# Kernel optimization log

Hardware: AMD Instinct MI355X
Metric: run time of the kernel (lower is better)

## Reference

```python
import jax, jax.numpy as jnp
import numpy as np

NUM_EMBEDS = 8192
EMBED_DIM = 256
BETA = 0.25


def setup_inputs() -> dict:
    key = jax.random.key(0)
    k1, k2 = jax.random.split(key)
    x_latent = jax.random.normal(k1, (16, EMBED_DIM, 32, 32), dtype=jnp.float32)
    # torch init: uniform(-1/num_embeds, 1/num_embeds)
    codebook = jax.random.uniform(
        k2, (NUM_EMBEDS, EMBED_DIM), dtype=jnp.float32,
        minval=-1.0 / NUM_EMBEDS, maxval=1.0 / NUM_EMBEDS)
    return {"x_latent": x_latent, "codebook": codebook}


def reference(x_latent, codebook):
    B, C, H, W = x_latent.shape  # C == EMBED_DIM
    # b c h w -> b (h w) c
    xf = x_latent.reshape(B, C, H * W).transpose(0, 2, 1)  # [B, N, D]
    x2 = jnp.sum(xf * xf, axis=-1, keepdims=True)            # [B, N, 1]
    e2 = jnp.sum(codebook * codebook, axis=-1)               # [E]
    xe = jnp.einsum('bnd,ed->bne', xf, codebook)             # [B, N, E]
    dist = x2 + e2[None, None, :] - 2.0 * xe
    encoding_inds = jnp.argmin(dist, axis=-1)                # [B, N] int
    quantized = jnp.take(codebook, encoding_inds, axis=0)    # [B, N, D]
    # b (h w) d -> b d h w
    quantized = quantized.transpose(0, 2, 1).reshape(B, C, H, W)
    commitment_loss = jnp.mean((jax.lax.stop_gradient(quantized) - x_latent) ** 2)
    embedding_loss = jnp.mean((quantized - jax.lax.stop_gradient(x_latent)) ** 2)
    vq_loss = commitment_loss * BETA + embedding_loss
    # straight-through estimator
    quantized_st = x_latent + jax.lax.stop_gradient(quantized - x_latent)
    return (quantized_st, vq_loss)
```

## Files before the change

kernel.cpp:

```cpp
#include <hip/hip_runtime.h>
#include <hip/hip_bf16.h>

typedef int   i4v  __attribute__((ext_vector_type(4)));
typedef int   i8v  __attribute__((ext_vector_type(8)));
typedef float f16v __attribute__((ext_vector_type(16)));

#define NUM_EMBEDS 8192
#define EMBED_DIM  256
#define BATCH      16
#define HW         1024
#define NVEC       (BATCH * HW)
#define OUT0_ELEMS (BATCH * EMBED_DIM * HW)
#define NSPLIT     8
#define COLS_PER_S 1024
#define NTILES     32

#define BUFB  8192
#define E2L   24576
#define SMEM3 28672

#define SCORE_BIAS 2097152.0f
#define SCALE_ONE 0x7F7F7F7F

#define WS_XQ   0
#define WS_EQ   4194304
#define WS_E2   6291456
#define WS_AMIN 6324224

static __device__ __forceinline__ void gload_lds16(const void* g, void* l) {
    __builtin_amdgcn_global_load_lds(
        (const __attribute__((address_space(1))) unsigned int*)g,
        (__attribute__((address_space(3))) unsigned int*)l, 16, 0, 0);
}

static __device__ __forceinline__ unsigned pk_fp8x4(float a, float b, float c, float d) {
    int w = __builtin_amdgcn_cvt_pk_fp8_f32(a, b, 0, false);
    w = __builtin_amdgcn_cvt_pk_fp8_f32(c, d, w, true);
    return (unsigned)w;
}

__global__ void k_prep(const float* __restrict__ x, const float* __restrict__ cb,
                       unsigned char* __restrict__ xq, unsigned char* __restrict__ eq,
                       float* __restrict__ e2, unsigned long long* __restrict__ amin,
                       float* __restrict__ out) {
    const int tx = threadIdx.x;
    const int ty = threadIdx.y;
    const int tid = ty * 32 + tx;

    if (blockIdx.z == 16) {
        const int bid = blockIdx.y * 32 + blockIdx.x;
        const int row = bid * 32 + (tid >> 3);
        const int sub = tid & 7;
        const float4* src = reinterpret_cast<const float4*>(cb + (size_t)row * 256 + sub * 32);
        float s = 0.f;
        unsigned ou[8];
        #pragma unroll
        for (int i = 0; i < 4; ++i) {
            const float4 a = src[2 * i], b = src[2 * i + 1];
            s = fmaf(a.x, a.x, s); s = fmaf(a.y, a.y, s);
            s = fmaf(a.z, a.z, s); s = fmaf(a.w, a.w, s);
            s = fmaf(b.x, b.x, s); s = fmaf(b.y, b.y, s);
            s = fmaf(b.z, b.z, s); s = fmaf(b.w, b.w, s);
            ou[2 * i]     = pk_fp8x4(a.x * 8192.f, a.y * 8192.f, a.z * 8192.f, a.w * 8192.f);
            ou[2 * i + 1] = pk_fp8x4(b.x * 8192.f, b.y * 8192.f, b.z * 8192.f, b.w * 8192.f);
        }
        uint4* dst = reinterpret_cast<uint4*>(eq + (size_t)row * 256 + sub * 32);
        dst[0] = make_uint4(ou[0], ou[1], ou[2], ou[3]);
        dst[1] = make_uint4(ou[4], ou[5], ou[6], ou[7]);
        s += __shfl_xor(s, 1, 64);
        s += __shfl_xor(s, 2, 64);
        s += __shfl_xor(s, 4, 64);
        if (sub == 0) e2[row] = fmaf(s, 67108864.0f, SCORE_BIAS);
        return;
    }

    __shared__ float t[32][33];
    const int hw0 = blockIdx.x * 32;
    const int c0  = blockIdx.y * 32;
    const int b   = blockIdx.z;
    if (blockIdx.z == 0 && blockIdx.y < 2) {
        const int i = (blockIdx.y * 32 + blockIdx.x) * 256 + tid;
        amin[i] = ~0ULL;
        if (i == 0) out[OUT0_ELEMS] = 0.0f;
    }
    #pragma unroll
    for (int i = 0; i < 4; ++i) {
        const int c = c0 + ty + i * 8;
        t[ty + i * 8][tx] = x[((b * EMBED_DIM + c) << 10) + hw0 + tx];
    }
    __syncthreads();
    {
        const unsigned w = pk_fp8x4(t[ty * 4 + 0][tx], t[ty * 4 + 1][tx],
                                    t[ty * 4 + 2][tx], t[ty * 4 + 3][tx]);
        const int n = (b << 10) + hw0 + tx;
        *reinterpret_cast<unsigned*>(xq + (size_t)n * 256 + c0 + ty * 4) = w;
    }
}

__global__ void __launch_bounds__(256, 2)
k_argmin(const unsigned char* __restrict__ xq, const unsigned char* __restrict__ eq,
         const float* __restrict__ e2, unsigned long long* __restrict__ amin) {
    extern __shared__ char smem[];
    const int tid  = threadIdx.x;
    const int lane = tid & 63;
    const int w    = tid >> 6;
    const int l31  = lane & 31;
    const int hi   = lane >> 5;
    const int s    = blockIdx.x & 7;
    const int rb   = blockIdx.x >> 3;
    const int row0 = rb * 256;
    const int cb0  = s * COLS_PER_S;

    const char* xqB = (const char*)xq;
    const char* eqB = (const char*)eq;
    const char* e2B = (const char*)e2;

    i8v afr[2][4];
    #pragma unroll
    for (int mr = 0; mr < 2; ++mr) {
        const int arow = row0 + w * 64 + mr * 32 + l31;
        const char* ap = xqB + ((size_t)arow << 8) + hi * 32;
        #pragma unroll
        for (int ks = 0; ks < 4; ++ks) {
            const i4v lo  = *reinterpret_cast<const i4v*>(ap + ks * 64);
            const i4v hi4 = *reinterpret_cast<const i4v*>(ap + ks * 64 + 16);
            afr[mr][ks] = (i8v){lo.x, lo.y, lo.z, lo.w, hi4.x, hi4.y, hi4.z, hi4.w};
        }
    }

    gload_lds16(e2B + ((size_t)cb0 << 2) + w * 1024 + lane * 16,
                smem + E2L + w * 1024);

    auto STAGE = [&](int tci, int lds_off) {
        #pragma unroll
        for (int j = 0; j < 2; ++j) {
            const int p = w * 2 + j;
            const int r = 4 * p + (lane >> 4);
            const int c = (lane & 15) ^ (r & 7);
            gload_lds16(eqB + ((size_t)(cb0 + tci * 32 + r) << 8) + (c << 4),
                        smem + lds_off + p * 1024);
        }
    };
    STAGE(0, 0);
    STAGE(1, BUFB);

    #pragma unroll
    for (int mr = 0; mr < 2; ++mr)
        #pragma unroll
        for (int ks = 0; ks < 4; ++ks)
            asm volatile("" : "+v"(afr[mr][ks]));

    unsigned mu0[16], mu1[16];
    #pragma unroll
    for (int r = 0; r < 16; ++r) { mu0[r] = 0xFFFFFFFFu; mu1[r] = 0xFFFFFFFFu; }

    const int sx = l31 & 7;

    auto PHASE = [&](int t, f16v& c0v, f16v& c1v, float& evS, unsigned& orvS) {
        if (t < NTILES - 1) {
            asm volatile("s_waitcnt vmcnt(2)" ::: "memory");
        } else {
            asm volatile("s_waitcnt vmcnt(0)" ::: "memory");
        }
        __builtin_amdgcn_s_barrier();
        if (t + 2 < NTILES) STAGE(t + 2, ((t + 2) % 3) * BUFB);

        evS  = *reinterpret_cast<const float*>(smem + E2L + t * 128 + l31 * 4);
        orvS = (unsigned)((t << 5) | l31);
        const char* bb = smem + (t % 3) * BUFB + l31 * 256;

        c0v = (f16v){}; c1v = (f16v){};
        __builtin_amdgcn_s_setprio(1);
        #pragma unroll
        for (int ks = 0; ks < 4; ++ks) {
            const int cc0 = (4 * ks + 2 * hi) ^ sx;
            const int cc1 = (4 * ks + 2 * hi + 1) ^ sx;
            const i4v lo  = *reinterpret_cast<const i4v*>(bb + (cc0 << 4));
            const i4v hi4 = *reinterpret_cast<const i4v*>(bb + (cc1 << 4));
            const i8v bf = (i8v){lo.x, lo.y, lo.z, lo.w, hi4.x, hi4.y, hi4.z, hi4.w};
            c0v = __builtin_amdgcn_mfma_scale_f32_32x32x64_f8f6f4(
                      afr[0][ks], bf, c0v, 0, 0, 0, SCALE_ONE, 0, SCALE_ONE);
            c1v = __builtin_amdgcn_mfma_scale_f32_32x32x64_f8f6f4(
                      afr[1][ks], bf, c1v, 0, 0, 0, SCALE_ONE, 0, SCALE_ONE);
        }
        __builtin_amdgcn_s_setprio(0);
    };

    auto EPI = [&](const f16v& c0v, const f16v& c1v, float evS, unsigned orvS) {
        #pragma unroll
        for (int r = 0; r < 16; ++r) {
            const float s0 = fmaf(-16384.0f, c0v[r], evS);
            mu0[r] = min(mu0[r], (__float_as_uint(s0) & 0xFFFFFC00u) | orvS);
            const float s1 = fmaf(-16384.0f, c1v[r], evS);
            mu1[r] = min(mu1[r], (__float_as_uint(s1) & 0xFFFFFC00u) | orvS);
        }
    };

    f16v aA0, aA1, aB0, aB1;
    float evA, evB; unsigned orvA, orvB;
    PHASE(0, aA0, aA1, evA, orvA);
    for (int t = 1; t < NTILES - 1; t += 2) {
        PHASE(t,     aB0, aB1, evB, orvB);  EPI(aA0, aA1, evA, orvA);
        PHASE(t + 1, aA0, aA1, evA, orvA);  EPI(aB0, aB1, evB, orvB);
    }
    PHASE(NTILES - 1, aB0, aB1, evB, orvB);
    EPI(aA0, aA1, evA, orvA);
    EPI(aB0, aB1, evB, orvB);

    #pragma unroll
    for (int mr = 0; mr < 2; ++mr)
        #pragma unroll
        for (int r = 0; r < 16; ++r) {
            unsigned u = mr ? mu1[r] : mu0[r];
            #pragma unroll
            for (int m = 1; m <= 16; m <<= 1)
                u = min(u, (unsigned)__shfl_xor((int)u, m, 64));
            if (l31 == 0) {
                const int row_g = row0 + w * 64 + mr * 32 + (r & 3) + 8 * (r >> 2) + 4 * hi;
                const int col = cb0 + (int)(u & 1023u);
                const unsigned long long key = ((unsigned long long)u << 32) | (unsigned)col;
                atomicMin(&amin[row_g], key);
            }
        }
}

__global__ void __launch_bounds__(256)
k_gather_loss(const float* __restrict__ x, const float* __restrict__ cb,
              const unsigned long long* __restrict__ amin, float* __restrict__ out) {
    __shared__ float q[32][257];
    __shared__ int e_s[32];
    const int tid = threadIdx.x;
    const int hw0 = (blockIdx.x & 31) * 32;
    const int b   = blockIdx.x >> 5;
    const int n0  = (b << 10) + hw0;
    if (tid < 32) e_s[tid] = (int)(amin[n0 + tid] & 0xFFFFFFFFu);
    __syncthreads();
    #pragma unroll 8
    for (int r = 0; r < 32; ++r)
        q[r][tid] = cb[(size_t)e_s[r] * EMBED_DIM + tid];
    __syncthreads();
    const int tx = tid & 31;
    const int ty = tid >> 5;
    float sum = 0.f;
    #pragma unroll
    for (int i = 0; i < 32; ++i) {
        const int c = ty * 32 + i;
        const float qv = q[tx][c];
        const int o = ((b * EMBED_DIM + c) << 10) + hw0 + tx;
        const float xv = x[o];
        out[o] = qv;
        const float d = qv - xv;
        sum = fmaf(d, d, sum);
    }
    #pragma unroll
    for (int off = 32; off > 0; off >>= 1) sum += __shfl_down(sum, off, 64);
    __shared__ float ls[4];
    const int lane = tid & 63, wid = tid >> 6;
    if (lane == 0) ls[wid] = sum;
    __syncthreads();
    if (tid == 0)
        atomicAdd(out + OUT0_ELEMS,
                  (ls[0] + ls[1] + ls[2] + ls[3]) * (1.25f / (float)OUT0_ELEMS));
}

extern "C" void kernel_launch(void* const* d_in, const int* in_sizes, int n_in,
                              void* d_out, int out_size, void* d_ws, size_t ws_size,
                              hipStream_t stream) {
    const float* x  = (const float*)d_in[0];
    const float* cb = (const float*)d_in[1];
    float* out = (float*)d_out;

    char* ws = (char*)d_ws;
    unsigned char* xq = (unsigned char*)(ws + WS_XQ);
    unsigned char* eq = (unsigned char*)(ws + WS_EQ);
    float* e2 = (float*)(ws + WS_E2);
    unsigned long long* amin = (unsigned long long*)(ws + WS_AMIN);

    k_prep<<<dim3(32, 8, 17), dim3(32, 8, 1), 0, stream>>>(x, cb, xq, eq, e2, amin, out);
    k_argmin<<<dim3(64 * NSPLIT), dim3(256), SMEM3, stream>>>(xq, eq, e2, amin);
    k_gather_loss<<<dim3(512), dim3(256), 0, stream>>>(x, cb, amin, out);
}
```

Before: 64.88 us.

## Pre-swizzle codebook into MFMA fragment layout and load B directly from global

The prep kernel now writes the fp8 codebook in a layout where each 32-column tile's MFMA B fragments sit contiguously per lane. The argmin kernel drops the LDS triple-buffer, barriers and global_load_lds staging, and instead loads B fragments and e2 values straight into registers, double-buffered in software one tile ahead. This removes LDS traffic and block-wide barriers. In exchange, all four waves in a block now fetch the same tile separately from global memory, relying on L2/L1 hits, and the extra B registers raise register pressure.

Result: slower. 102.9 us (+58.6%).

```diff
diff --git a/kernel.cpp b/kernel.cpp
--- a/kernel.cpp
+++ b/kernel.cpp
@@ -15,10 +15,6 @@
 #define COLS_PER_S 1024
 #define NTILES     32
 
-#define BUFB  8192
-#define E2L   24576
-#define SMEM3 28672
-
 #define SCORE_BIAS 2097152.0f
 #define SCALE_ONE 0x7F7F7F7F
 
@@ -27,12 +23,6 @@
 #define WS_E2   6291456
 #define WS_AMIN 6324224
 
-static __device__ __forceinline__ void gload_lds16(const void* g, void* l) {
-    __builtin_amdgcn_global_load_lds(
-        (const __attribute__((address_space(1))) unsigned int*)g,
-        (__attribute__((address_space(3))) unsigned int*)l, 16, 0, 0);
-}
-
 static __device__ __forceinline__ unsigned pk_fp8x4(float a, float b, float c, float d) {
     int w = __builtin_amdgcn_cvt_pk_fp8_f32(a, b, 0, false);
     w = __builtin_amdgcn_cvt_pk_fp8_f32(c, d, w, true);
@@ -40,7 +30,7 @@
 }
 
 __global__ void k_prep(const float* __restrict__ x, const float* __restrict__ cb,
-                       unsigned char* __restrict__ xq, unsigned char* __restrict__ eq,
+                       unsigned char* __restrict__ xq, unsigned char* __restrict__ eqF,
                        float* __restrict__ e2, unsigned long long* __restrict__ amin,
                        float* __restrict__ out) {
     const int tx = threadIdx.x;
@@ -64,7 +54,9 @@
             ou[2 * i]     = pk_fp8x4(a.x * 8192.f, a.y * 8192.f, a.z * 8192.f, a.w * 8192.f);
             ou[2 * i + 1] = pk_fp8x4(b.x * 8192.f, b.y * 8192.f, b.z * 8192.f, b.w * 8192.f);
         }
-        uint4* dst = reinterpret_cast<uint4*>(eq + (size_t)row * 256 + sub * 32);
+        const size_t off = ((size_t)(row >> 5) * 4 + (sub >> 1)) * 2048
+                         + (((sub & 1) << 5) | (row & 31)) * 32;
+        uint4* dst = reinterpret_cast<uint4*>(eqF + off);
         dst[0] = make_uint4(ou[0], ou[1], ou[2], ou[3]);
         dst[1] = make_uint4(ou[4], ou[5], ou[6], ou[7]);
         s += __shfl_xor(s, 1, 64);
@@ -98,9 +90,8 @@
 }
 
 __global__ void __launch_bounds__(256, 2)
-k_argmin(const unsigned char* __restrict__ xq, const unsigned char* __restrict__ eq,
+k_argmin(const unsigned char* __restrict__ xq, const unsigned char* __restrict__ eqF,
          const float* __restrict__ e2, unsigned long long* __restrict__ amin) {
-    extern __shared__ char smem[];
     const int tid  = threadIdx.x;
     const int lane = tid & 63;
     const int w    = tid >> 6;
@@ -112,8 +103,7 @@
     const int cb0  = s * COLS_PER_S;
 
     const char* xqB = (const char*)xq;
-    const char* eqB = (const char*)eq;
-    const char* e2B = (const char*)e2;
+    const char* eqB = (const char*)eqF;
 
     i8v afr[2][4];
     #pragma unroll
@@ -127,23 +117,6 @@
             afr[mr][ks] = (i8v){lo.x, lo.y, lo.z, lo.w, hi4.x, hi4.y, hi4.z, hi4.w};
         }
     }
-
-    gload_lds16(e2B + ((size_t)cb0 << 2) + w * 1024 + lane * 16,
-                smem + E2L + w * 1024);
-
-    auto STAGE = [&](int tci, int lds_off) {
-        #pragma unroll
-        for (int j = 0; j < 2; ++j) {
-            const int p = w * 2 + j;
-            const int r = 4 * p + (lane >> 4);
-            const int c = (lane & 15) ^ (r & 7);
-            gload_lds16(eqB + ((size_t)(cb0 + tci * 32 + r) << 8) + (c << 4),
-                        smem + lds_off + p * 1024);
-        }
-    };
-    STAGE(0, 0);
-    STAGE(1, BUFB);
-
     #pragma unroll
     for (int mr = 0; mr < 2; ++mr)
         #pragma unroll
@@ -154,34 +127,26 @@
     #pragma unroll
     for (int r = 0; r < 16; ++r) { mu0[r] = 0xFFFFFFFFu; mu1[r] = 0xFFFFFFFFu; }
 
-    const int sx = l31 & 7;
-
-    auto PHASE = [&](int t, f16v& c0v, f16v& c1v, float& evS, unsigned& orvS) {
-        if (t < NTILES - 1) {
-            asm volatile("s_waitcnt vmcnt(2)" ::: "memory");
-        } else {
-            asm volatile("s_waitcnt vmcnt(0)" ::: "memory");
-        }
-        __builtin_amdgcn_s_barrier();
-        if (t + 2 < NTILES) STAGE(t + 2, ((t + 2) % 3) * BUFB);
-
-        evS  = *reinterpret_cast<const float*>(smem + E2L + t * 128 + l31 * 4);
-        orvS = (unsigned)((t << 5) | l31);
-        const char* bb = smem + (t % 3) * BUFB + l31 * 256;
-
+    auto LOADT = [&](int t, i8v* B, float& ev) {
+        const char* bp = eqB + ((size_t)((s * 32 + t) * 4) * 2048) + lane * 32;
+        #pragma unroll
+        for (int ks = 0; ks < 4; ++ks) {
+            const i4v lo  = *reinterpret_cast<const i4v*>(bp + ks * 2048);
+            const i4v hi4 = *reinterpret_cast<const i4v*>(bp + ks * 2048 + 16);
+            B[ks] = (i8v){lo.x, lo.y, lo.z, lo.w, hi4.x, hi4.y, hi4.z, hi4.w};
+        }
+        ev = e2[cb0 + t * 32 + l31];
+    };
+
+    auto BURST = [&](const i8v* B, f16v& c0v, f16v& c1v) {
         c0v = (f16v){}; c1v = (f16v){};
         __builtin_amdgcn_s_setprio(1);
         #pragma unroll
         for (int ks = 0; ks < 4; ++ks) {
-            const int cc0 = (4 * ks + 2 * hi) ^ sx;
-            const int cc1 = (4 * ks + 2 * hi + 1) ^ sx;
-            const i4v lo  = *reinterpret_cast<const i4v*>(bb + (cc0 << 4));
-            const i4v hi4 = *reinterpret_cast<const i4v*>(bb + (cc1 << 4));
-            const i8v bf = (i8v){lo.x, lo.y, lo.z, lo.w, hi4.x, hi4.y, hi4.z, hi4.w};
             c0v = __builtin_amdgcn_mfma_scale_f32_32x32x64_f8f6f4(
-                      afr[0][ks], bf, c0v, 0, 0, 0, SCALE_ONE, 0, SCALE_ONE);
+                      afr[0][ks], B[ks], c0v, 0, 0, 0, SCALE_ONE, 0, SCALE_ONE);
             c1v = __builtin_amdgcn_mfma_scale_f32_32x32x64_f8f6f4(
-                      afr[1][ks], bf, c1v, 0, 0, 0, SCALE_ONE, 0, SCALE_ONE);
+                      afr[1][ks], B[ks], c1v, 0, 0, 0, SCALE_ONE, 0, SCALE_ONE);
         }
         __builtin_amdgcn_s_setprio(0);
     };
@@ -196,16 +161,29 @@
         }
     };
 
-    f16v aA0, aA1, aB0, aB1;
-    float evA, evB; unsigned orvA, orvB;
-    PHASE(0, aA0, aA1, evA, orvA);
+    i8v BA[4], BB[4];
+    float evLa, evLb;
+    f16v xA0, xA1, yB0, yB1;
+    float evX, evY; unsigned orvX, orvY;
+
+    LOADT(0, BA, evLa);
+    LOADT(1, BB, evLb);
+    evX = evLa; orvX = (unsigned)((0 << 5) | l31);
+    BURST(BA, xA0, xA1);
     for (int t = 1; t < NTILES - 1; t += 2) {
-        PHASE(t,     aB0, aB1, evB, orvB);  EPI(aA0, aA1, evA, orvA);
-        PHASE(t + 1, aA0, aA1, evA, orvA);  EPI(aB0, aB1, evB, orvB);
-    }
-    PHASE(NTILES - 1, aB0, aB1, evB, orvB);
-    EPI(aA0, aA1, evA, orvA);
-    EPI(aB0, aB1, evB, orvB);
+        LOADT(t + 1, BA, evLa);
+        evY = evLb; orvY = (unsigned)((t << 5) | l31);
+        BURST(BB, yB0, yB1);
+        EPI(xA0, xA1, evX, orvX);
+        LOADT(t + 2, BB, evLb);
+        evX = evLa; orvX = (unsigned)(((t + 1) << 5) | l31);
+        BURST(BA, xA0, xA1);
+        EPI(yB0, yB1, evY, orvY);
+    }
+    evY = evLb; orvY = (unsigned)(((NTILES - 1) << 5) | l31);
+    BURST(BB, yB0, yB1);
+    EPI(xA0, xA1, evX, orvX);
+    EPI(yB0, yB1, evY, orvY);
 
     #pragma unroll
     for (int mr = 0; mr < 2; ++mr)
@@ -272,11 +250,11 @@
 
     char* ws = (char*)d_ws;
     unsigned char* xq = (unsigned char*)(ws + WS_XQ);
-    unsigned char* eq = (unsigned char*)(ws + WS_EQ);
+    unsigned char* eqF = (unsigned char*)(ws + WS_EQ);
     float* e2 = (float*)(ws + WS_E2);
     unsigned long long* amin = (unsigned long long*)(ws + WS_AMIN);
 
-    k_prep<<<dim3(32, 8, 17), dim3(32, 8, 1), 0, stream>>>(x, cb, xq, eq, e2, amin, out);
-    k_argmin<<<dim3(64 * NSPLIT), dim3(256), SMEM3, stream>>>(xq, eq, e2, amin);
+    k_prep<<<dim3(32, 8, 17), dim3(32, 8, 1), 0, stream>>>(x, cb, xq, eqF, e2, amin, out);
+    k_argmin<<<dim3(64 * NSPLIT), dim3(256), 0, stream>>>(xq, eqF, e2, amin);
     k_gather_loss<<<dim3(512), dim3(256), 0, stream>>>(x, cb, amin, out);
 }
```
